# Kernel optimization log

Measured on AMD Instinct MI355X. Metric: run time of the kernel, lower is better.

The kernel has to match this reference:

```python
import jax, jax.numpy as jnp
import numpy as np
from jax import lax

EPS = 1e-8
QB = 127.0  # 2**(8-1) - 1
LN_EPS = 1e-5

B, S, E, D = 32, 4096, 64, 32


def _ste(x, q):
    return x + lax.stop_gradient(q - x)


def _bitlinear(x, w, b):
    # BitLinear158b: ternary absmean weight quant + 8-bit absmax activation quant (STE)
    beta = jnp.maximum(jnp.mean(jnp.abs(w)), EPS)
    wq = jnp.clip(jnp.round(w / beta), -1.0, 1.0) * beta
    gamma = QB / jnp.maximum(jnp.max(jnp.abs(x), axis=-1, keepdims=True), EPS)
    xq = jnp.clip(jnp.round(x * gamma), -(QB + 1.0), QB) / gamma
    return _ste(x, xq) @ _ste(w, wq).T + b


def _layernorm(x, g, b):
    m = jnp.mean(x, axis=-1, keepdims=True)
    v = jnp.mean(jnp.square(x - m), axis=-1, keepdims=True)
    return (x - m) * lax.rsqrt(v + LN_EPS) * g + b


def _conv3x3(x, w, b):
    y = lax.conv_general_dilated(x, w, (1, 1), 'SAME',
                                 dimension_numbers=('NCHW', 'OIHW', 'NCHW'))
    return y + b.reshape(1, -1, 1, 1)


def _gelu(x):
    return jax.nn.gelu(x, approximate=False)


def setup_inputs() -> dict:
    key = jax.random.key(0)
    ks = jax.random.split(key, 20)
    d = {
        'x': jax.random.normal(ks[0], (B, S, E), jnp.float32),
        'interact2': jax.random.normal(ks[1], (B, D, D), jnp.float32),
        'qw': jax.random.normal(ks[2], (E, E), jnp.float32) * 0.05,
        'qb': jnp.zeros((E,), jnp.float32),
        'kw': jax.random.normal(ks[3], (E, E), jnp.float32) * 0.05,
        'kb': jnp.zeros((E,), jnp.float32),
        'vw': jax.random.normal(ks[4], (E, E), jnp.float32) * 0.05,
        'vb': jnp.zeros((E,), jnp.float32),
        'f1w': jax.random.normal(ks[5], (E, E), jnp.float32) * 0.05,
        'f1b': jnp.zeros((E,), jnp.float32),
        'f2w': jax.random.normal(ks[6], (E, E), jnp.float32) * 0.05,
        'f2b': jnp.zeros((E,), jnp.float32),
        'c1w': jax.random.normal(ks[7], (1, 1, 3, 3), jnp.float32) * 0.2,
        'c1b': jnp.zeros((1,), jnp.float32),
        'c2w': jax.random.normal(ks[8], (1, 1, 3, 3), jnp.float32) * 0.2,
        'c2b': jnp.zeros((1,), jnp.float32),
        'c3w': jax.random.normal(ks[9], (1, 1, 3, 3), jnp.float32) * 0.2,
        'c3b': jnp.zeros((1,), jnp.float32),
        'ln1g': jnp.ones((E,), jnp.float32), 'ln1b': jnp.zeros((E,), jnp.float32),
        'ln2g': jnp.ones((E,), jnp.float32), 'ln2b': jnp.zeros((E,), jnp.float32),
        'ln3g': jnp.ones((E,), jnp.float32), 'ln3b': jnp.zeros((E,), jnp.float32),
        'ln4g': jnp.ones((E,), jnp.float32), 'ln4b': jnp.zeros((E,), jnp.float32),
    }
    return d


def reference(x, interact2, qw, qb, kw, kb, vw, vb, f1w, f1b, f2w, f2b,
              c1w, c1b, c2w, c2b, c3w, c3b,
              ln1g, ln1b, ln2g, ln2b, ln3g, ln3b, ln4g, ln4b):
    residual1 = x
    b, s, e = x.shape
    xn = _layernorm(x, ln1g, ln1b)
    # NOTE: .view(B, E, S) is a raw reinterpret of the (B,S,E) buffer, not a transpose
    q = _bitlinear(xn, qw, qb).reshape(b, e, s)
    k = _bitlinear(xn, kw, kb).reshape(b, e, s)
    v = _bitlinear(xn, vw, vb).reshape(b, e, s)

    it = interact2[:, None, :, :]
    it = jax.image.resize(it, (b, 1, 64, 64), method='linear')  # align_corners=False
    it = _gelu(_conv3x3(it, c1w, c1b))  # dropout4: identity (eval)
    it = _gelu(_conv3x3(it, c2w, c2b))
    it = _gelu(_conv3x3(it, c3w, c3b))
    it = it[:, 0]  # (B, 64, 64)

    scale = jnp.sqrt(jnp.float32(e))
    scores = jnp.einsum('bes,bfs->bef', q, k) / scale + it  # (B,E,E)
    attn = jax.nn.softmax(scores, axis=-1)
    out = jnp.einsum('bef,bfs->bes', attn, v)  # (B,E,S)
    out = jnp.transpose(out, (0, 2, 1)).reshape(b, s, e)
    out = out - xn  # dropout: identity (eval)
    out = _layernorm(out, ln2g, ln2b)
    residual2 = out + residual1
    out = _layernorm(out + residual1, ln3g, ln3b)
    out = _gelu(_bitlinear(out, f1w, f1b))
    out = _layernorm(out, ln4g, ln4b)
    out = _bitlinear(out, f2w, f2b)
    return out + residual2
```

## Files before the change

### kernel.cpp

```cpp
#include <hip/hip_runtime.h>

#define EPSQ 1e-8f
#define QBC  127.0f
#define LNE  1e-5f

typedef float f32x4 __attribute__((ext_vector_type(4)));

#if defined(__has_builtin)
#  if __has_builtin(__builtin_amdgcn_sdot4)
#    define SDOT4(a,b,c) __builtin_amdgcn_sdot4((a),(b),(c),false)
#  endif
#endif
#ifndef SDOT4
__device__ __forceinline__ int sdot4_sw(int a, int b, int c){
  c += ((a<<24)>>24) * ((b<<24)>>24);
  c += ((a<<16)>>24) * ((b<<16)>>24);
  c += ((a<< 8)>>24) * ((b<< 8)>>24);
  c += ( a>>24     ) * ( b>>24     );
  return c;
}
#  define SDOT4(a,b,c) sdot4_sw((a),(b),(c))
#endif

constexpr size_t OFF_WPK  = 0;
constexpr size_t OFF_BETA = 20480;
constexpr size_t OFF_IG   = 20544;
constexpr size_t OFF_MR   = OFF_IG + 524288;
constexpr size_t OFF_Q    = OFF_MR + 1048576;
constexpr size_t OFF_K    = OFF_Q  + 16777216;
constexpr size_t OFF_V    = OFF_K  + 16777216;
constexpr size_t OFF_SC   = OFF_V  + 16777216;

__device__ __forceinline__ float gelu_f(float v){
  return 0.5f * v * (1.0f + erff(v * 0.70710678118654752f));
}
__device__ __forceinline__ int pack4(float q0, float q1, float q2, float q3){
  return ((int)q0 & 255) | (((int)q1 & 255) << 8) | (((int)q2 & 255) << 16) | (((int)q3 & 255) << 24);
}

__global__ __launch_bounds__(1024) void k_prep(
    const float* qw, const float* kw, const float* vw, const float* f1w, const float* f2w,
    const float* it2, const float* c1w, const float* c1b, const float* c2w, const float* c2b,
    const float* c3w, const float* c3b, int* __restrict__ wpk, float* __restrict__ beta5,
    float* __restrict__ sco){
  __shared__ float smem[1024 + 2*64*65];
  int t = threadIdx.x;
  if (blockIdx.x < 5){
    int m = blockIdx.x;
    const float* w = (m==0)?qw:(m==1)?kw:(m==2)?vw:(m==3)?f1w:f2w;
    float* red = smem;
    float s = 0.f;
    for (int i = t; i < 4096; i += 1024) s += fabsf(w[i]);
    red[t] = s; __syncthreads();
    for (int o = 512; o > 0; o >>= 1){ if (t < o) red[t] += red[t+o]; __syncthreads(); }
    float beta = fmaxf(red[0] * (1.0f/4096.0f), EPSQ);
    if (t == 0) beta5[m] = beta;
    int* dst = wpk + m*1024;
    if (t < 1024){
      int row = t >> 4, kp = t & 15;
      int v = 0;
      #pragma unroll
      for (int j = 0; j < 4; j++){
        float q = rintf(w[row*64 + kp*4 + j] / beta);
        q = fminf(fmaxf(q, -1.f), 1.f);
        v |= ((int)q & 255) << (8*j);
      }
      dst[t] = v;
    }
  } else {
    int b = blockIdx.x - 5;
    float* in32 = smem;
    float (*Aa)[65] = (float(*)[65])(smem + 1024);
    float (*Bb)[65] = (float(*)[65])(smem + 1024 + 64*65);
    for (int i = t; i < 1024; i += 1024) in32[i] = it2[b*1024 + i];
    __syncthreads();
    for (int p = t; p < 4096; p += 1024){
      int i = p >> 6, j = p & 63;
      float si = 0.5f*i - 0.25f, fi = floorf(si), wi = si - fi;
      int i0 = min(max((int)fi, 0), 31), i1 = min(max((int)fi + 1, 0), 31);
      float sj = 0.5f*j - 0.25f, fj = floorf(sj), wj = sj - fj;
      int j0 = min(max((int)fj, 0), 31), j1 = min(max((int)fj + 1, 0), 31);
      float v00 = in32[i0*32+j0], v01 = in32[i0*32+j1];
      float v10 = in32[i1*32+j0], v11 = in32[i1*32+j1];
      Aa[i][j] = (1.f-wi)*((1.f-wj)*v00 + wj*v01) + wi*((1.f-wj)*v10 + wj*v11);
    }
    __syncthreads();
    {
      float w9[9]; for (int q2=0;q2<9;q2++) w9[q2]=c1w[q2]; float bb = c1b[0];
      for (int p = t; p < 4096; p += 1024){
        int i = p>>6, j = p&63; float s = bb;
        #pragma unroll
        for (int di=-1; di<=1; di++)
          #pragma unroll
          for (int dj=-1; dj<=1; dj++){
            int ii=i+di, jj=j+dj;
            if (ii>=0 && ii<64 && jj>=0 && jj<64) s += w9[(di+1)*3+dj+1]*Aa[ii][jj];
          }
        Bb[i][j] = gelu_f(s);
      }
    }
    __syncthreads();
    {
      float w9[9]; for (int q2=0;q2<9;q2++) w9[q2]=c2w[q2]; float bb = c2b[0];
      for (int p = t; p < 4096; p += 1024){
        int i = p>>6, j = p&63; float s = bb;
        #pragma unroll
        for (int di=-1; di<=1; di++)
          #pragma unroll
          for (int dj=-1; dj<=1; dj++){
            int ii=i+di, jj=j+dj;
            if (ii>=0 && ii<64 && jj>=0 && jj<64) s += w9[(di+1)*3+dj+1]*Bb[ii][jj];
          }
        Aa[i][j] = gelu_f(s);
      }
    }
    __syncthreads();
    {
      float w9[9]; for (int q2=0;q2<9;q2++) w9[q2]=c3w[q2]; float bb = c3b[0];
      for (int p = t; p < 4096; p += 1024){
        int i = p>>6, j = p&63; float s = bb;
        #pragma unroll
        for (int di=-1; di<=1; di++)
          #pragma unroll
          for (int dj=-1; dj<=1; dj++){
            int ii=i+di, jj=j+dj;
            if (ii>=0 && ii<64 && jj>=0 && jj<64) s += w9[(di+1)*3+dj+1]*Aa[ii][jj];
          }
        sco[b*4096 + p] = gelu_f(s);
      }
    }
  }
}

__global__ __launch_bounds__(256,4) void k_qkv(const float* __restrict__ x,
    const float* __restrict__ ln1g, const float* __restrict__ ln1b,
    const int* __restrict__ wpk, float2* __restrict__ mr, float* __restrict__ ig,
    short* __restrict__ q16, short* __restrict__ k16, short* __restrict__ v16){
  __shared__ int Wp[3][64][17];
  __shared__ int Xp[64][17];
  int t = threadIdx.x;
  for (int i = t; i < 3072; i += 256){
    int m = i >> 10, rem = i & 1023;
    Wp[m][rem>>4][rem&15] = wpk[i];
  }
  int c = t >> 2, g = t & 3;
  long n = (long)blockIdx.x * 64 + c;
  const float* xr = x + n*64 + g*16;
  float xv[16];
  #pragma unroll
  for (int i4 = 0; i4 < 4; i4++){
    float4 f = ((const float4*)xr)[i4];
    xv[4*i4+0]=f.x; xv[4*i4+1]=f.y; xv[4*i4+2]=f.z; xv[4*i4+3]=f.w;
  }
  float s = 0.f;
  #pragma unroll
  for (int i = 0; i < 16; i++) s += xv[i];
  s += __shfl_xor(s,1); s += __shfl_xor(s,2);
  float mean = s * (1.0f/64.0f);
  float vs = 0.f;
  #pragma unroll
  for (int i = 0; i < 16; i++){ float dd = xv[i]-mean; vs += dd*dd; }
  vs += __shfl_xor(vs,1); vs += __shfl_xor(vs,2);
  float rs = rsqrtf(vs*(1.0f/64.0f) + LNE);
  float xnv[16]; float amax = 0.f;
  #pragma unroll
  for (int i = 0; i < 16; i++){
    float u = (xv[i]-mean)*rs*ln1g[g*16+i] + ln1b[g*16+i];
    xnv[i] = u; amax = fmaxf(amax, fabsf(u));
  }
  amax = fmaxf(amax, __shfl_xor(amax,1)); amax = fmaxf(amax, __shfl_xor(amax,2));
  float am = fmaxf(amax, EPSQ);
  float gamma = QBC / am;
  if (g == 0){ ig[n] = am * (1.0f/QBC); mr[n] = make_float2(mean, rs); }
  #pragma unroll
  for (int i4 = 0; i4 < 4; i4++){
    float q0 = fminf(fmaxf(rintf(xnv[4*i4+0]*gamma), -128.f), 127.f);
    float q1 = fminf(fmaxf(rintf(xnv[4*i4+1]*gamma), -128.f), 127.f);
    float q2 = fminf(fmaxf(rintf(xnv[4*i4+2]*gamma), -128.f), 127.f);
    float q3 = fminf(fmaxf(rintf(xnv[4*i4+3]*gamma), -128.f), 127.f);
    Xp[c][g*4+i4] = pack4(q0,q1,q2,q3);
  }
  __syncthreads();

  int r0 = (t >> 4) << 2, c0 = (t & 15) << 2;
  #pragma unroll
  for (int m = 0; m < 3; m++){
    int acc[4][4] = {};
    #pragma unroll
    for (int kp = 0; kp < 16; kp++){
      int av[4], bv[4];
      #pragma unroll
      for (int i = 0; i < 4; i++) av[i] = Xp[r0+i][kp];
      #pragma unroll
      for (int j = 0; j < 4; j++) bv[j] = Wp[m][c0+j][kp];
      #pragma unroll
      for (int i = 0; i < 4; i++)
        #pragma unroll
        for (int j = 0; j < 4; j++)
          acc[i][j] = SDOT4(av[i], bv[j], acc[i][j]);
    }
    short* op = ((m==0)?q16:(m==1)?k16:v16) + (long)blockIdx.x*4096;
    #pragma unroll
    for (int i = 0; i < 4; i++){
      short4 s4;
      s4.x = (short)acc[i][0]; s4.y = (short)acc[i][1];
      s4.z = (short)acc[i][2]; s4.w = (short)acc[i][3];
      *(short4*)&op[(r0+i)*64 + c0] = s4;
    }
  }
}

__global__ __launch_bounds__(256,4) void k_qk(
    const short* __restrict__ q16, const short* __restrict__ k16,
    const float* __restrict__ ig, const float* __restrict__ beta5,
    const float* __restrict__ qbias, const float* __restrict__ kbias,
    float* __restrict__ sco){
  __shared__ float Qs[64][68];
  __shared__ float Kt[64][68];
  __shared__ float qbs[64], kbs[64];
  int t = threadIdx.x;
  int b = blockIdx.x >> 5, ch = blockIdx.x & 31;
  int c = t >> 2, g = t & 3;
  int r0 = (t >> 4) << 2, c0 = (t & 15) << 2;
  if (t < 64){ qbs[t] = qbias[t]; kbs[t] = kbias[t]; }
  float bq = beta5[0], bk = beta5[1];
  const short* qbase = q16 + (long)b*262144 + (long)c*4096;
  const short* kbase = k16 + (long)b*262144 + (long)c*4096;
  float acc[4][4] = {};
  for (int sub = 0; sub < 2; sub++){
    int t0 = ch*128 + sub*64 + g*16;
    int4 qa = *(const int4*)(qbase + t0);
    int4 qb2 = *(const int4*)(qbase + t0 + 8);
    int4 ka = *(const int4*)(kbase + t0);
    int4 kb2 = *(const int4*)(kbase + t0 + 8);
    float sgi = ig[b*4096 + c*64 + ch*2 + sub];
    float sq = bq * sgi, sk = bk * sgi;
    __syncthreads();
    int qi[8] = {qa.x,qa.y,qa.z,qa.w,qb2.x,qb2.y,qb2.z,qb2.w};
    int ki[8] = {ka.x,ka.y,ka.z,ka.w,kb2.x,kb2.y,kb2.z,kb2.w};
    #pragma unroll
    for (int w2 = 0; w2 < 8; w2++){
      int e0 = g*16 + 2*w2, e1 = e0 + 1;
      Qs[c][e0] = (float)((qi[w2]<<16)>>16)*sq + qbs[e0];
      Qs[c][e1] = (float)( qi[w2]>>16      )*sq + qbs[e1];
      Kt[e0][c] = (float)((ki[w2]<<16)>>16)*sk + kbs[e0];
      Kt[e1][c] = (float)( ki[w2]>>16      )*sk + kbs[e1];
    }
    __syncthreads();
    for (int k4 = 0; k4 < 64; k4 += 4){
      float4 a[4], bv[4];
      #pragma unroll
      for (int i = 0; i < 4; i++) a[i] = *(const float4*)&Qs[r0+i][k4];
      #pragma unroll
      for (int kk = 0; kk < 4; kk++) bv[kk] = *(const float4*)&Kt[k4+kk][c0];
      #pragma unroll
      for (int i = 0; i < 4; i++){
        const float* ap = (const float*)&a[i];
        #pragma unroll
        for (int kk = 0; kk < 4; kk++){
          float av = ap[kk];
          acc[i][0] = fmaf(av, bv[kk].x, acc[i][0]);
          acc[i][1] = fmaf(av, bv[kk].y, acc[i][1]);
          acc[i][2] = fmaf(av, bv[kk].z, acc[i][2]);
          acc[i][3] = fmaf(av, bv[kk].w, acc[i][3]);
        }
      }
    }
  }
  float* sc = sco + b*4096;
  #pragma unroll
  for (int i = 0; i < 4; i++)
    #pragma unroll
    for (int j = 0; j < 4; j++)
      atomicAdd(&sc[(r0+i)*64 + c0 + j], acc[i][j]*0.125f);
}

__global__ __launch_bounds__(256,3) void k_epi(const float* __restrict__ x,
    const short* __restrict__ v16, const float* __restrict__ sco,
    const float2* __restrict__ mr, const float* __restrict__ ig,
    const float* __restrict__ beta5, const int* __restrict__ wpk,
    const float* ln1g, const float* ln1b,
    const float* ln2g, const float* ln2b, const float* ln3g, const float* ln3b,
    const float* ln4g, const float* ln4b, const float* __restrict__ vbias,
    const float* f1b, const float* f2b, float* __restrict__ out){
  __shared__ float B1[64][68];
  __shared__ float B2[64][68];
  __shared__ int Wp[2][64][17];
  __shared__ int Xp[64][17];
  __shared__ float gam1[64], gam2[64];
  int t = threadIdx.x;
  int b = blockIdx.x >> 6;
  int s0 = (blockIdx.x & 63) << 6;
  float bv_ = beta5[2];
  for (int i = t; i < 4096; i += 256){
    int r = i >> 6, cc = i & 63;
    B1[r][cc] = sco[b*4096 + i];
    float sv = bv_ * ig[b*4096 + r*64 + (s0 >> 6)];
    B2[r][cc] = (float)v16[(long)b*262144 + (long)r*4096 + s0 + cc] * sv + vbias[cc];
  }
  for (int i = t; i < 2048; i += 256){
    int m = i >> 10, rem = i & 1023;
    Wp[m][rem>>4][rem&15] = wpk[(3+m)*1024 + rem];
  }
  __syncthreads();
  int c = t >> 2, g = t & 3;
  {
    float sv[16];
    #pragma unroll
    for (int i4 = 0; i4 < 4; i4++){
      float4 f = *(const float4*)&B1[c][g*16 + 4*i4];
      sv[4*i4+0]=f.x; sv[4*i4+1]=f.y; sv[4*i4+2]=f.z; sv[4*i4+3]=f.w;
    }
    float mx = sv[0];
    #pragma unroll
    for (int i = 1; i < 16; i++) mx = fmaxf(mx, sv[i]);
    mx = fmaxf(mx, __shfl_xor(mx,1)); mx = fmaxf(mx, __shfl_xor(mx,2));
    float se = 0.f;
    #pragma unroll
    for (int i = 0; i < 16; i++){ sv[i] = expf(sv[i]-mx); se += sv[i]; }
    se += __shfl_xor(se,1); se += __shfl_xor(se,2);
    float inv = 1.0f/se;
    #pragma unroll
    for (int i4 = 0; i4 < 4; i4++)
      *(float4*)&B1[c][g*16+4*i4] = make_float4(sv[4*i4]*inv, sv[4*i4+1]*inv, sv[4*i4+2]*inv, sv[4*i4+3]*inv);
  }
  __syncthreads();
  int r0 = (t >> 4) << 2, c0 = (t & 15) << 2;
  float acc[4][4] = {};
  for (int k4 = 0; k4 < 64; k4 += 4){
    float4 a[4], bv[4];
    #pragma unroll
    for (int i = 0; i < 4; i++) a[i] = *(const float4*)&B1[r0+i][k4];
    #pragma unroll
    for (int kk = 0; kk < 4; kk++) bv[kk] = *(const float4*)&B2[k4+kk][c0];
    #pragma unroll
    for (int i = 0; i < 4; i++){
      const float* ap = (const float*)&a[i];
      #pragma unroll
      for (int kk = 0; kk < 4; kk++){
        float av = ap[kk];
        acc[i][0] = fmaf(av, bv[kk].x, acc[i][0]);
        acc[i][1] = fmaf(av, bv[kk].y, acc[i][1]);
        acc[i][2] = fmaf(av, bv[kk].z, acc[i][2]);
        acc[i][3] = fmaf(av, bv[kk].w, acc[i][3]);
      }
    }
  }
  __syncthreads();
  #pragma unroll
  for (int i = 0; i < 4; i++)
    #pragma unroll
    for (int j = 0; j < 4; j++) B1[c0+j][r0+i] = acc[i][j];
  __syncthreads();
  long n = (long)b*4096 + s0 + c;
  const float* xp = x + n*64 + g*16;
  float xa[16];
  #pragma unroll
  for (int i4 = 0; i4 < 4; i4++){
    float4 f = ((const float4*)xp)[i4];
    xa[4*i4+0]=f.x; xa[4*i4+1]=f.y; xa[4*i4+2]=f.z; xa[4*i4+3]=f.w;
  }
  float2 m2 = mr[n];
  float d[16];
  #pragma unroll
  for (int i4 = 0; i4 < 4; i4++){
    float4 f = *(const float4*)&B1[c][g*16 + 4*i4];
    d[4*i4+0]=f.x; d[4*i4+1]=f.y; d[4*i4+2]=f.z; d[4*i4+3]=f.w;
  }
  #pragma unroll
  for (int i = 0; i < 16; i++){
    float xn_i = (xa[i]-m2.x)*m2.y*ln1g[g*16+i] + ln1b[g*16+i];
    d[i] -= xn_i;
  }
  float s = 0.f;
  #pragma unroll
  for (int i = 0; i < 16; i++) s += d[i];
  s += __shfl_xor(s,1); s += __shfl_xor(s,2);
  float mean = s*(1.0f/64.0f);
  float vs = 0.f;
  #pragma unroll
  for (int i = 0; i < 16; i++){ float dd = d[i]-mean; vs += dd*dd; }
  vs += __shfl_xor(vs,1); vs += __shfl_xor(vs,2);
  float rs = rsqrtf(vs*(1.0f/64.0f) + LNE);
  float r2[16];
  #pragma unroll
  for (int i = 0; i < 16; i++){
    float t2 = (d[i]-mean)*rs*ln2g[g*16+i] + ln2b[g*16+i];
    r2[i] = t2 + xa[i];
  }
  #pragma unroll
  for (int i4 = 0; i4 < 4; i4++)
    *(float4*)&B2[c][g*16+4*i4] = make_float4(r2[4*i4],r2[4*i4+1],r2[4*i4+2],r2[4*i4+3]);
  s = 0.f;
  #pragma unroll
  for (int i = 0; i < 16; i++) s += r2[i];
  s += __shfl_xor(s,1); s += __shfl_xor(s,2);
  float mean3 = s*(1.0f/64.0f);
  vs = 0.f;
  #pragma unroll
  for (int i = 0; i < 16; i++){ float dd = r2[i]-mean3; vs += dd*dd; }
  vs += __shfl_xor(vs,1); vs += __shfl_xor(vs,2);
  float rs3 = rsqrtf(vs*(1.0f/64.0f) + LNE);
  float u16v[16]; float amax = 0.f;
  #pragma unroll
  for (int i = 0; i < 16; i++){
    float u = (r2[i]-mean3)*rs3*ln3g[g*16+i] + ln3b[g*16+i];
    u16v[i] = u; amax = fmaxf(amax, fabsf(u));
  }
  amax = fmaxf(amax, __shfl_xor(amax,1)); amax = fmaxf(amax, __shfl_xor(amax,2));
  float gamma = QBC / fmaxf(amax, EPSQ);
  #pragma unroll
  for (int i4 = 0; i4 < 4; i4++){
    float q0 = fminf(fmaxf(rintf(u16v[4*i4+0]*gamma), -128.f), 127.f);
    float q1 = fminf(fmaxf(rintf(u16v[4*i4+1]*gamma), -128.f), 127.f);
    float q2 = fminf(fmaxf(rintf(u16v[4*i4+2]*gamma), -128.f), 127.f);
    float q3 = fminf(fmaxf(rintf(u16v[4*i4+3]*gamma), -128.f), 127.f);
    Xp[c][g*4+i4] = pack4(q0,q1,q2,q3);
  }
  if (g == 0) gam1[c] = gamma;
  __syncthreads();
  int ac2[4][4] = {};
  #pragma unroll
  for (int kp = 0; kp < 16; kp++){
    int av[4], bv2[4];
    #pragma unroll
    for (int i = 0; i < 4; i++) av[i] = Xp[r0+i][kp];
    #pragma unroll
    for (int j = 0; j < 4; j++) bv2[j] = Wp[0][c0+j][kp];
    #pragma unroll
    for (int i = 0; i < 4; i++)
      #pragma unroll
      for (int j = 0; j < 4; j++)
        ac2[i][j] = SDOT4(av[i], bv2[j], ac2[i][j]);
  }
  __syncthreads();
  float beta1 = beta5[3], beta2 = beta5[4];
  #pragma unroll
  for (int i = 0; i < 4; i++){
    float sc = beta1 / gam1[r0+i];
    #pragma unroll
    for (int j = 0; j < 4; j++)
      B1[r0+i][c0+j] = gelu_f((float)ac2[i][j]*sc + f1b[c0+j]);
  }
  __syncthreads();
  float gl[16];
  #pragma unroll
  for (int i4 = 0; i4 < 4; i4++){
    float4 f = *(const float4*)&B1[c][g*16 + 4*i4];
    gl[4*i4+0]=f.x; gl[4*i4+1]=f.y; gl[4*i4+2]=f.z; gl[4*i4+3]=f.w;
  }
  s = 0.f;
  #pragma unroll
  for (int i = 0; i < 16; i++) s += gl[i];
  s += __shfl_xor(s,1); s += __shfl_xor(s,2);
  float mean4 = s*(1.0f/64.0f);
  vs = 0.f;
  #pragma unroll
  for (int i = 0; i < 16; i++){ float dd = gl[i]-mean4; vs += dd*dd; }
  vs += __shfl_xor(vs,1); vs += __shfl_xor(vs,2);
  float rs4 = rsqrtf(vs*(1.0f/64.0f) + LNE);
  amax = 0.f;
  #pragma unroll
  for (int i = 0; i < 16; i++){
    float u = (gl[i]-mean4)*rs4*ln4g[g*16+i] + ln4b[g*16+i];
    u16v[i] = u; amax = fmaxf(amax, fabsf(u));
  }
  amax = fmaxf(amax, __shfl_xor(amax,1)); amax = fmaxf(amax, __shfl_xor(amax,2));
  float gamma2 = QBC / fmaxf(amax, EPSQ);
  #pragma unroll
  for (int i4 = 0; i4 < 4; i4++){
    float q0 = fminf(fmaxf(rintf(u16v[4*i4+0]*gamma2), -128.f), 127.f);
    float q1 = fminf(fmaxf(rintf(u16v[4*i4+1]*gamma2), -128.f), 127.f);
    float q2 = fminf(fmaxf(rintf(u16v[4*i4+2]*gamma2), -128.f), 127.f);
    float q3 = fminf(fmaxf(rintf(u16v[4*i4+3]*gamma2), -128.f), 127.f);
    Xp[c][g*4+i4] = pack4(q0,q1,q2,q3);
  }
  if (g == 0) gam2[c] = gamma2;
  __syncthreads();
  int ac3[4][4] = {};
  #pragma unroll
  for (int kp = 0; kp < 16; kp++){
    int av[4], bv2[4];
    #pragma unroll
    for (int i = 0; i < 4; i++) av[i] = Xp[r0+i][kp];
    #pragma unroll
    for (int j = 0; j < 4; j++) bv2[j] = Wp[1][c0+j][kp];
    #pragma unroll
    for (int i = 0; i < 4; i++)
      #pragma unroll
      for (int j = 0; j < 4; j++)
        ac3[i][j] = SDOT4(av[i], bv2[j], ac3[i][j]);
  }
  float4 bf = *(const float4*)&f2b[c0];
  #pragma unroll
  for (int i = 0; i < 4; i++){
    float sc = beta2 / gam2[r0+i];
    float4 rr = *(const float4*)&B2[r0+i][c0];
    f32x4 o;
    o.x = (float)ac3[i][0]*sc + bf.x + rr.x;
    o.y = (float)ac3[i][1]*sc + bf.y + rr.y;
    o.z = (float)ac3[i][2]*sc + bf.z + rr.z;
    o.w = (float)ac3[i][3]*sc + bf.w + rr.w;
    __builtin_nontemporal_store(o, (f32x4*)&out[((long)b*4096 + s0 + r0 + i)*64 + c0]);
  }
}

extern "C" void kernel_launch(void* const* d_in, const int* in_sizes, int n_in,
                              void* d_out, int out_size, void* d_ws, size_t ws_size,
                              hipStream_t stream){
  const float* x    = (const float*)d_in[0];
  const float* it2  = (const float*)d_in[1];
  const float* qw   = (const float*)d_in[2];
  const float* qb   = (const float*)d_in[3];
  const float* kw   = (const float*)d_in[4];
  const float* kb   = (const float*)d_in[5];
  const float* vw   = (const float*)d_in[6];
  const float* vb   = (const float*)d_in[7];
  const float* f1w  = (const float*)d_in[8];
  const float* f1b  = (const float*)d_in[9];
  const float* f2w  = (const float*)d_in[10];
  const float* f2b  = (const float*)d_in[11];
  const float* c1w  = (const float*)d_in[12];
  const float* c1b  = (const float*)d_in[13];
  const float* c2w  = (const float*)d_in[14];
  const float* c2b  = (const float*)d_in[15];
  const float* c3w  = (const float*)d_in[16];
  const float* c3b  = (const float*)d_in[17];
  const float* ln1g = (const float*)d_in[18];
  const float* ln1b = (const float*)d_in[19];
  const float* ln2g = (const float*)d_in[20];
  const float* ln2b = (const float*)d_in[21];
  const float* ln3g = (const float*)d_in[22];
  const float* ln3b = (const float*)d_in[23];
  const float* ln4g = (const float*)d_in[24];
  const float* ln4b = (const float*)d_in[25];
  float* out = (float*)d_out;

  char* w = (char*)d_ws;
  int*    wpk   = (int*)(w + OFF_WPK);
  float*  beta5 = (float*)(w + OFF_BETA);
  float*  ig    = (float*)(w + OFF_IG);
  float2* mr    = (float2*)(w + OFF_MR);
  short*  q16   = (short*)(w + OFF_Q);
  short*  k16   = (short*)(w + OFF_K);
  short*  v16   = (short*)(w + OFF_V);
  float*  sco   = (float*)(w + OFF_SC);

  hipLaunchKernelGGL(k_prep, dim3(37),   dim3(1024), 0, stream,
                     qw, kw, vw, f1w, f2w, it2, c1w, c1b, c2w, c2b, c3w, c3b, wpk, beta5, sco);
  hipLaunchKernelGGL(k_qkv,  dim3(2048), dim3(256), 0, stream,
                     x, ln1g, ln1b, wpk, mr, ig, q16, k16, v16);
  hipLaunchKernelGGL(k_qk,   dim3(1024), dim3(256), 0, stream,
                     q16, k16, ig, beta5, qb, kb, sco);
  hipLaunchKernelGGL(k_epi,  dim3(2048), dim3(256), 0, stream,
                     x, v16, sco, mr, ig, beta5, wpk, ln1g, ln1b,
                     ln2g, ln2b, ln3g, ln3b, ln4g, ln4b, vb, f1b, f2b, out);
}
```

Before: 321.8 us.

## Replace atomic score reduction with partials plus a dedicated softmax reduce kernel

After: 269.8 us. -16.1%, faster.

```diff
diff --git a/kernel.cpp b/kernel.cpp
--- a/kernel.cpp
+++ b/kernel.cpp
@@ -30,6 +30,7 @@
 constexpr size_t OFF_K    = OFF_Q  + 16777216;
 constexpr size_t OFF_V    = OFF_K  + 16777216;
 constexpr size_t OFF_SC   = OFF_V  + 16777216;
+constexpr size_t OFF_SP   = OFF_SC + 524288;
 
 __device__ __forceinline__ float gelu_f(float v){
   return 0.5f * v * (1.0f + erff(v * 0.70710678118654752f));
@@ -132,7 +133,7 @@
   }
 }
 
-__global__ __launch_bounds__(256,4) void k_qkv(const float* __restrict__ x,
+__global__ __launch_bounds__(256,2) void k_qkv(const float* __restrict__ x,
     const float* __restrict__ ln1g, const float* __restrict__ ln1b,
     const int* __restrict__ wpk, float2* __restrict__ mr, float* __restrict__ ig,
     short* __restrict__ q16, short* __restrict__ k16, short* __restrict__ v16){
@@ -210,16 +211,16 @@
   }
 }
 
-__global__ __launch_bounds__(256,4) void k_qk(
+__global__ __launch_bounds__(256,2) void k_qk(
     const short* __restrict__ q16, const short* __restrict__ k16,
     const float* __restrict__ ig, const float* __restrict__ beta5,
     const float* __restrict__ qbias, const float* __restrict__ kbias,
-    float* __restrict__ sco){
+    float* __restrict__ sp){
   __shared__ float Qs[64][68];
   __shared__ float Kt[64][68];
   __shared__ float qbs[64], kbs[64];
   int t = threadIdx.x;
-  int b = blockIdx.x >> 5, ch = blockIdx.x & 31;
+  int b = blockIdx.x >> 4, ch = blockIdx.x & 15;
   int c = t >> 2, g = t & 3;
   int r0 = (t >> 4) << 2, c0 = (t & 15) << 2;
   if (t < 64){ qbs[t] = qbias[t]; kbs[t] = kbias[t]; }
@@ -227,13 +228,13 @@
   const short* qbase = q16 + (long)b*262144 + (long)c*4096;
   const short* kbase = k16 + (long)b*262144 + (long)c*4096;
   float acc[4][4] = {};
-  for (int sub = 0; sub < 2; sub++){
-    int t0 = ch*128 + sub*64 + g*16;
+  for (int sub = 0; sub < 4; sub++){
+    int t0 = ch*256 + sub*64 + g*16;
     int4 qa = *(const int4*)(qbase + t0);
     int4 qb2 = *(const int4*)(qbase + t0 + 8);
     int4 ka = *(const int4*)(kbase + t0);
     int4 kb2 = *(const int4*)(kbase + t0 + 8);
-    float sgi = ig[b*4096 + c*64 + ch*2 + sub];
+    float sgi = ig[b*4096 + c*64 + ch*4 + sub];
     float sq = bq * sgi, sk = bk * sgi;
     __syncthreads();
     int qi[8] = {qa.x,qa.y,qa.z,qa.w,qb2.x,qb2.y,qb2.z,qb2.w};
@@ -267,15 +268,35 @@
       }
     }
   }
-  float* sc = sco + b*4096;
-  #pragma unroll
-  for (int i = 0; i < 4; i++)
-    #pragma unroll
-    for (int j = 0; j < 4; j++)
-      atomicAdd(&sc[(r0+i)*64 + c0 + j], acc[i][j]*0.125f);
-}
-
-__global__ __launch_bounds__(256,3) void k_epi(const float* __restrict__ x,
+  float* spo = sp + ((long)b*16 + ch)*4096;
+  #pragma unroll
+  for (int i = 0; i < 4; i++){
+    f32x4 o; o.x = acc[i][0]*0.125f; o.y = acc[i][1]*0.125f;
+    o.z = acc[i][2]*0.125f; o.w = acc[i][3]*0.125f;
+    *(f32x4*)&spo[(r0+i)*64 + c0] = o;
+  }
+}
+
+__global__ __launch_bounds__(256) void k_rsm(const float* __restrict__ sp, float* __restrict__ sco){
+  int row = blockIdx.x*4 + (threadIdx.x >> 6);
+  int lane = threadIdx.x & 63;
+  int b = row >> 6, e = row & 63;
+  long off = (long)b*4096 + e*64 + lane;
+  float v = sco[off];
+  const float* spp = sp + (long)b*65536 + e*64 + lane;
+  #pragma unroll
+  for (int ch = 0; ch < 16; ch++) v += spp[ch*4096];
+  float mx = v;
+  #pragma unroll
+  for (int o = 1; o < 64; o <<= 1) mx = fmaxf(mx, __shfl_xor(mx, o));
+  float ev = expf(v - mx);
+  float sum = ev;
+  #pragma unroll
+  for (int o = 1; o < 64; o <<= 1) sum += __shfl_xor(sum, o);
+  sco[off] = ev / sum;
+}
+
+__global__ __launch_bounds__(256,4) void k_epi(const float* __restrict__ x,
     const short* __restrict__ v16, const float* __restrict__ sco,
     const float2* __restrict__ mr, const float* __restrict__ ig,
     const float* __restrict__ beta5, const int* __restrict__ wpk,
@@ -285,7 +306,6 @@
     const float* f1b, const float* f2b, float* __restrict__ out){
   __shared__ float B1[64][68];
   __shared__ float B2[64][68];
-  __shared__ int Wp[2][64][17];
   __shared__ int Xp[64][17];
   __shared__ float gam1[64], gam2[64];
   int t = threadIdx.x;
@@ -298,33 +318,8 @@
     float sv = bv_ * ig[b*4096 + r*64 + (s0 >> 6)];
     B2[r][cc] = (float)v16[(long)b*262144 + (long)r*4096 + s0 + cc] * sv + vbias[cc];
   }
-  for (int i = t; i < 2048; i += 256){
-    int m = i >> 10, rem = i & 1023;
-    Wp[m][rem>>4][rem&15] = wpk[(3+m)*1024 + rem];
-  }
   __syncthreads();
   int c = t >> 2, g = t & 3;
-  {
-    float sv[16];
-    #pragma unroll
-    for (int i4 = 0; i4 < 4; i4++){
-      float4 f = *(const float4*)&B1[c][g*16 + 4*i4];
-      sv[4*i4+0]=f.x; sv[4*i4+1]=f.y; sv[4*i4+2]=f.z; sv[4*i4+3]=f.w;
-    }
-    float mx = sv[0];
-    #pragma unroll
-    for (int i = 1; i < 16; i++) mx = fmaxf(mx, sv[i]);
-    mx = fmaxf(mx, __shfl_xor(mx,1)); mx = fmaxf(mx, __shfl_xor(mx,2));
-    float se = 0.f;
-    #pragma unroll
-    for (int i = 0; i < 16; i++){ sv[i] = expf(sv[i]-mx); se += sv[i]; }
-    se += __shfl_xor(se,1); se += __shfl_xor(se,2);
-    float inv = 1.0f/se;
-    #pragma unroll
-    for (int i4 = 0; i4 < 4; i4++)
-      *(float4*)&B1[c][g*16+4*i4] = make_float4(sv[4*i4]*inv, sv[4*i4+1]*inv, sv[4*i4+2]*inv, sv[4*i4+3]*inv);
-  }
-  __syncthreads();
   int r0 = (t >> 4) << 2, c0 = (t & 15) << 2;
   float acc[4][4] = {};
   for (int k4 = 0; k4 < 64; k4 += 4){
@@ -419,6 +414,7 @@
   }
   if (g == 0) gam1[c] = gamma;
   __syncthreads();
+  const int* w1 = wpk + 3*1024;
   int ac2[4][4] = {};
   #pragma unroll
   for (int kp = 0; kp < 16; kp++){
@@ -426,7 +422,7 @@
     #pragma unroll
     for (int i = 0; i < 4; i++) av[i] = Xp[r0+i][kp];
     #pragma unroll
-    for (int j = 0; j < 4; j++) bv2[j] = Wp[0][c0+j][kp];
+    for (int j = 0; j < 4; j++) bv2[j] = w1[(c0+j)*16 + kp];
     #pragma unroll
     for (int i = 0; i < 4; i++)
       #pragma unroll
@@ -477,6 +473,7 @@
   }
   if (g == 0) gam2[c] = gamma2;
   __syncthreads();
+  const int* w2 = wpk + 4*1024;
   int ac3[4][4] = {};
   #pragma unroll
   for (int kp = 0; kp < 16; kp++){
@@ -484,7 +481,7 @@
     #pragma unroll
     for (int i = 0; i < 4; i++) av[i] = Xp[r0+i][kp];
     #pragma unroll
-    for (int j = 0; j < 4; j++) bv2[j] = Wp[1][c0+j][kp];
+    for (int j = 0; j < 4; j++) bv2[j] = w2[(c0+j)*16 + kp];
     #pragma unroll
     for (int i = 0; i < 4; i++)
       #pragma unroll
@@ -545,13 +542,15 @@
   short*  k16   = (short*)(w + OFF_K);
   short*  v16   = (short*)(w + OFF_V);
   float*  sco   = (float*)(w + OFF_SC);
+  float*  sp    = (float*)(w + OFF_SP);
 
   hipLaunchKernelGGL(k_prep, dim3(37),   dim3(1024), 0, stream,
                      qw, kw, vw, f1w, f2w, it2, c1w, c1b, c2w, c2b, c3w, c3b, wpk, beta5, sco);
   hipLaunchKernelGGL(k_qkv,  dim3(2048), dim3(256), 0, stream,
                      x, ln1g, ln1b, wpk, mr, ig, q16, k16, v16);
-  hipLaunchKernelGGL(k_qk,   dim3(1024), dim3(256), 0, stream,
-                     q16, k16, ig, beta5, qb, kb, sco);
+  hipLaunchKernelGGL(k_qk,   dim3(512),  dim3(256), 0, stream,
+                     q16, k16, ig, beta5, qb, kb, sp);
+  hipLaunchKernelGGL(k_rsm,  dim3(512),  dim3(256), 0, stream, sp, sco);
   hipLaunchKernelGGL(k_epi,  dim3(2048), dim3(256), 0, stream,
                      x, v16, sco, mr, ig, beta5, wpk, ln1g, ln1b,
                      ln2g, ln2b, ln3g, ln3b, ln4g, ln4b, vb, f1b, f2b, out);
```
